# Kernel optimization log

Hardware: AMD Instinct MI355X
Metric: run time of the kernel (lower is better)

The kernel has to match this reference:

```python
import jax, jax.numpy as jnp
import numpy as np

VOCAB, EMBED, TOPICS, NDOCS = 30000, 200, 100, 2048
DT_ALPHA, TW_ALPHA = 3.0, 2.0
EPS_OT = 1e-16   # ETP sinkhorn epsilon
EPS_LOG = 1e-12  # FASTopic self.epsilon
N_SINKHORN_ITERS = 100  # fixed iteration count (original: while err>thr and cpt<max_iter)


def pairwise_sqeuclidean(x, y):
    return (jnp.sum(x * x, axis=1, keepdims=True)
            + jnp.sum(y * y, axis=1)
            - 2.0 * (x @ y.T))


def sinkhorn_etp(x, y, a, b, alpha):
    # Entropic OT between point clouds x:[n,d], y:[m,d]; a:[n,1], b:[m,1] marginals.
    M = pairwise_sqeuclidean(x, y)          # [n, m]
    K = jnp.exp(-alpha * M)                  # Gibbs kernel
    u0 = jnp.full_like(a, 1.0 / a.shape[0])

    def step(carry, _):
        u, _v = carry
        v = b / (K.T @ u + EPS_OT)           # [m,1]
        u = a / (K @ v + EPS_OT)             # [n,1]
        return (u, v), None

    (u, v), _ = jax.lax.scan(step, (u0, jnp.zeros_like(b)), None, length=N_SINKHORN_ITERS)
    transp = u * (K * v.T)                   # [n, m] transport plan
    loss = jnp.sum(transp * M)
    return loss, transp


def setup_inputs() -> dict:
    key = jax.random.key(0)
    k1, k2, k3, k4 = jax.random.split(key, 4)
    # word_embeddings: trunc_normal(std=1) then L2-row-normalize
    we = jax.random.truncated_normal(k1, -2.0, 2.0, (VOCAB, EMBED), jnp.float32)
    we = we / jnp.linalg.norm(we, axis=1, keepdims=True)
    # topic_embeddings: trunc_normal(std=0.1) then L2-row-normalize
    te = 0.1 * jax.random.truncated_normal(k2, -2.0, 2.0, (TOPICS, EMBED), jnp.float32)
    te = te / jnp.linalg.norm(te, axis=1, keepdims=True)
    word_weights = jnp.full((VOCAB, 1), 1.0 / VOCAB, jnp.float32)
    topic_weights = jnp.full((TOPICS, 1), 1.0 / TOPICS, jnp.float32)
    train_bow = jax.random.uniform(k3, (NDOCS, VOCAB), jnp.float32)
    doc_embeddings = jax.random.normal(k4, (NDOCS, EMBED), jnp.float32)
    return {
        "train_bow": train_bow,
        "doc_embeddings": doc_embeddings,
        "word_embeddings": we,
        "topic_embeddings": te,
        "word_weights": word_weights,
        "topic_weights": topic_weights,
    }


def reference(train_bow, doc_embeddings, word_embeddings, topic_embeddings,
              word_weights, topic_weights):
    n_docs = doc_embeddings.shape[0]
    n_topics = topic_embeddings.shape[0]
    # DT_ETP: a uniform over docs, b = softmax(topic_weights)
    a_dt = jnp.full((n_docs, 1), 1.0 / n_docs, doc_embeddings.dtype)
    b_dt = jax.nn.softmax(topic_weights, axis=0)
    loss_DT, transp_DT = sinkhorn_etp(doc_embeddings, topic_embeddings, a_dt, b_dt, DT_ALPHA)
    # TW_ETP: a uniform over topics, b = softmax(word_weights)
    a_tw = jnp.full((n_topics, 1), 1.0 / n_topics, topic_embeddings.dtype)
    b_tw = jax.nn.softmax(word_weights, axis=0)
    loss_TW, transp_TW = sinkhorn_etp(topic_embeddings, word_embeddings, a_tw, b_tw, TW_ALPHA)

    loss_ETP = loss_DT + loss_TW
    theta = transp_DT * n_docs               # [N, K]
    beta = transp_TW * n_topics              # [K, V]
    recon = theta @ beta                     # [N, V]
    loss_DSR = -jnp.mean(jnp.sum(train_bow * jnp.log(recon + EPS_LOG), axis=1))
    loss = loss_DSR + loss_ETP
    return loss, loss_DSR, loss_ETP
```

## Files before the change

kernel.cpp:

```cpp
#include <hip/hip_runtime.h>
#include <math.h>

#define V 30000
#define E 200
#define T 100
#define N 2048
#define NITER 100
#define KSTR 112
#define EPS_OT 1e-16f
#define EPS_LOG 1e-12f

#define OFF_KTW    0
#define OFF_KDT    1680000
#define OFF_WW     1884800
#define OFF_DD     1914800
#define OFF_TT     1916848
#define OFF_PM     1916976
#define OFF_PS     1917104
#define OFF_BTW    1917232
#define OFF_BDT    1947232
#define OFF_ACC    1947360
#define OFF_ACCDT  1957360
#define OFF_VTW    1967360
#define OFF_UDT    1997360
#define OFF_UTW    1999408
#define OFF_VDT    1999536
#define OFF_DBL    1999664
#define OFF_FLAG   1999680
#define OFF_KDTNZ  1999681
#define OFF_ARR    1999682

#define NTW 118
#define NDT 8

#define LOBF(u) __uint_as_float((u) << 16)
#define HIBF(u) __uint_as_float((u) & 0xffff0000u)

__device__ __forceinline__ unsigned short f2bf(float f) {
    unsigned int u = __float_as_uint(f);
    return (unsigned short)((u + 0x7fffu + ((u >> 16) & 1u)) >> 16);
}
__device__ __forceinline__ float bf2f(unsigned short h) {
    return __uint_as_float(((unsigned int)h) << 16);
}

__device__ __forceinline__ float brsum(float x, float* red8) {
    int tid = threadIdx.x;
    for (int o = 32; o; o >>= 1) x += __shfl_down(x, o, 64);
    __syncthreads();
    if ((tid & 63) == 0) red8[tid >> 6] = x;
    __syncthreads();
    return (red8[0] + red8[1]) + (red8[2] + red8[3]);
}

__device__ __forceinline__ void load_krow(const unsigned short* kg, int j, unsigned* ku) {
    const uint4* kp = (const uint4*)(kg + (size_t)j * KSTR);
    #pragma unroll
    for (int i = 0; i < 12; i++) {
        uint4 q = kp[i];
        ku[4*i] = q.x; ku[4*i+1] = q.y; ku[4*i+2] = q.z; ku[4*i+3] = q.w;
    }
    uint2 q2 = *(const uint2*)(((const unsigned*)kp) + 48);
    ku[48] = q2.x; ku[49] = q2.y;
}

__device__ __forceinline__ void gbar(int* ctr, int n, int tid) {
    __syncthreads();
    if (tid == 0) {
        __hip_atomic_fetch_add(ctr, 1, __ATOMIC_RELEASE, __HIP_MEMORY_SCOPE_AGENT);
        while (__hip_atomic_load(ctr, __ATOMIC_ACQUIRE, __HIP_MEMORY_SCOPE_AGENT) < n)
            __builtin_amdgcn_s_sleep(1);
    }
    __syncthreads();
}

__device__ __forceinline__ float agent_ldf(const float* p) {
    return __hip_atomic_load(p, __ATOMIC_RELAXED, __HIP_MEMORY_SCOPE_AGENT);
}

__global__ void k_pre(const float* __restrict__ we, const float* __restrict__ de,
                      const float* __restrict__ te, const float* __restrict__ wwgt,
                      const float* __restrict__ twgt, float* ws) {
    __shared__ float red[256];
    int tid = threadIdx.x, b = blockIdx.x;
    int gid = b * 256 + tid;
    if (gid < 2 * NITER * T) ws[OFF_ACC + gid] = 0.f;
    if (gid < 16) ws[OFF_DBL + gid] = 0.f;
    if (gid < 2) ((int*)ws)[OFF_FLAG + gid] = 0;
    if (gid < 2 * NITER) ((int*)ws)[OFF_ARR + gid] = 0;
    {
        int r = gid;
        const float* src = nullptr; float* dst = nullptr; int row = 0;
        if (r < V)              { src = we; dst = ws + OFF_WW; row = r; }
        else if (r < V + N)     { src = de; dst = ws + OFF_DD; row = r - V; }
        else if (r < V + N + T) { src = te; dst = ws + OFF_TT; row = r - V - N; }
        if (src) {
            const float4* p = (const float4*)(src + (size_t)row * E);
            float s = 0.f;
            #pragma unroll 10
            for (int i = 0; i < E / 4; i++) { float4 v = p[i]; s += v.x*v.x + v.y*v.y + v.z*v.z + v.w*v.w; }
            dst[row] = s;
        }
    }
    if (b < 118) {
        int j = gid;
        float w = (j < V) ? wwgt[j] : -INFINITY;
        red[tid] = w; __syncthreads();
        for (int s = 128; s > 0; s >>= 1) { if (tid < s) red[tid] = fmaxf(red[tid], red[tid + s]); __syncthreads(); }
        float m = red[0]; __syncthreads();
        float e = (j < V) ? expf(w - m) : 0.f;
        red[tid] = e; __syncthreads();
        for (int s = 128; s > 0; s >>= 1) { if (tid < s) red[tid] += red[tid + s]; __syncthreads(); }
        if (tid == 0) { ws[OFF_PM + b] = m; ws[OFF_PS + b] = red[0]; }
    } else if (b == 120) {
        float w = (tid < T) ? twgt[tid] : -INFINITY;
        red[tid] = w; __syncthreads();
        for (int s = 128; s > 0; s >>= 1) { if (tid < s) red[tid] = fmaxf(red[tid], red[tid + s]); __syncthreads(); }
        float m = red[0]; __syncthreads();
        float e = (tid < T) ? expf(w - m) : 0.f;
        red[tid] = e; __syncthreads();
        for (int s = 128; s > 0; s >>= 1) { if (tid < s) red[tid] += red[tid + s]; __syncthreads(); }
        if (tid < T) ws[OFF_BDT + tid] = e / red[0];
    }
}

__global__ void k_pre2(const float* __restrict__ wwgt, float* ws) {
    __shared__ float red[128];
    int tid = threadIdx.x, b = blockIdx.x;
    float m = (tid < 118) ? ws[OFF_PM + tid] : -INFINITY;
    if (tid < 128) red[tid] = m;
    __syncthreads();
    for (int s = 64; s > 0; s >>= 1) { if (tid < s) red[tid] = fmaxf(red[tid], red[tid + s]); __syncthreads(); }
    float mw = red[0]; __syncthreads();
    float p = (tid < 118) ? ws[OFF_PS + tid] * expf(ws[OFF_PM + tid] - mw) : 0.f;
    if (tid < 128) red[tid] = p;
    __syncthreads();
    for (int s = 64; s > 0; s >>= 1) { if (tid < s) red[tid] += red[tid + s]; __syncthreads(); }
    float Sw = red[0];
    int j = b * 256 + tid;
    if (j < V) ws[OFF_BTW + j] = expf(wwgt[j] - mw) / Sw;
}

__global__ void k_ktw(const float* __restrict__ we, const float* __restrict__ te, float* ws) {
    __shared__ float wt[8][256];
    __shared__ float tp[8][25];
    __shared__ float tts[25];
    int tid = threadIdx.x;
    int j0 = blockIdx.x * 256;
    int t0 = blockIdx.y * 25;
    int j = j0 + tid;
    int jl = (j < V) ? j : V - 1;
    float acc[25];
    #pragma unroll
    for (int i = 0; i < 25; i++) acc[i] = 0.f;
    if (tid < 25) tts[tid] = ws[OFF_TT + t0 + tid];
    for (int kk = 0; kk < E; kk += 8) {
        #pragma unroll
        for (int k = 0; k < 8; k++) wt[k][tid] = we[(size_t)jl * E + kk + k];
        if (tid < 200) { int i = tid >> 3; int k = tid & 7; tp[k][i] = te[(size_t)(t0 + i) * E + kk + k]; }
        __syncthreads();
        #pragma unroll
        for (int k = 0; k < 8; k++) {
            float w = wt[k][tid];
            #pragma unroll
            for (int i = 0; i < 25; i++) acc[i] += tp[k][i] * w;
        }
        __syncthreads();
    }
    if (j < V) {
        float wwj = ws[OFF_WW + j];
        unsigned short* kg = (unsigned short*)(ws + OFF_KTW);
        #pragma unroll
        for (int i = 0; i < 25; i++) {
            float M = tts[i] + wwj - 2.f * acc[i];
            kg[(size_t)j * KSTR + t0 + i] = f2bf(expf(-2.f * M));
        }
    }
}

__global__ void k_kdt(const float* __restrict__ de, const float* __restrict__ te, float* ws) {
    int gid = blockIdx.x * 256 + threadIdx.x;
    if (gid >= N * T) return;
    int n = gid / T; int t = gid - n * T;
    const float4* dp  = (const float4*)(de + (size_t)n * E);
    const float4* tpp = (const float4*)(te + (size_t)t * E);
    float s = 0.f;
    #pragma unroll 10
    for (int i = 0; i < E / 4; i++) { float4 a = dp[i], b = tpp[i]; s += a.x*b.x + a.y*b.y + a.z*b.z + a.w*b.w; }
    float M = ws[OFF_DD + n] + ws[OFF_TT + t] - 2.f * s;
    float kv = expf(-3.f * M);
    ws[OFF_KDT + gid] = kv;
    unsigned long long m = __ballot(kv != 0.f);
    if (m && (threadIdx.x & 63) == 0) atomicOr(((int*)ws) + OFF_KDTNZ, 1);
}

__global__ __launch_bounds__(256, 1) void k_sink(const float* __restrict__ bow, float* ws) {
    __shared__ float sm[256 * 26];
    __shared__ float pr[256];
    __shared__ float u_sh[100];
    __shared__ float red8[8];
    int tid = threadIdx.x, b = blockIdx.x;
    int* arr = ((int*)ws) + OFF_ARR;

    if (b >= 118 && b < 246) {
        const float4* b4 = (const float4*)bow;
        for (int k = 0; k < 96; k++) {
            size_t base = (size_t)k * 160000;
            float s = 0.f;
            for (int i = (b - 118) * 256 + tid; i < 160000; i += 128 * 256) {
                float4 x = b4[base + i]; s += (x.x + x.y) + (x.z + x.w);
            }
            float bs = brsum(s, red8);
            if (tid == 0) atomicAdd((double*)(ws + OFF_DBL) + 3, (double)bs);
        }
        return;
    }

    if (b >= 246) {
        if (((volatile int*)ws)[OFF_KDTNZ] == 0) return;
        int d = (b - 246) * 256 + tid;
        const float* Kr = ws + OFF_KDT + (size_t)d * T;
        for (int k = 0; k < NITER; k++) {
            if (tid < T) u_sh[tid] = (k == 0) ? 0.f
                : ws[OFF_BDT + tid] / (agent_ldf(ws + OFF_ACCDT + (k - 1) * T + tid) + EPS_OT);
            __syncthreads();
            float u;
            if (k == 0) u = 1.f / N;
            else {
                float s = 0.f;
                #pragma unroll 4
                for (int t = 0; t < T; t++) s += Kr[t] * u_sh[t];
                u = (1.f / N) / (s + EPS_OT);
            }
            #pragma unroll
            for (int c = 0; c < 4; c++) {
                #pragma unroll
                for (int i = 0; i < 25; i++) sm[tid * 26 + i] = Kr[25 * c + i] * u;
                __syncthreads();
                int g = tid >> 5, tl = tid & 31;
                float s2 = 0.f;
                if (tl < 25) {
                    #pragma unroll 8
                    for (int q = 0; q < 32; q++) s2 += sm[(g * 32 + q) * 26 + tl];
                }
                pr[g * 32 + tl] = s2;
                __syncthreads();
                if (tid < 25) {
                    float r = 0.f;
                    #pragma unroll
                    for (int g2 = 0; g2 < 8; g2++) r += pr[g2 * 32 + tid];
                    atomicAdd(&ws[OFF_ACCDT + k * T + 25 * c + tid], r);
                }
                __syncthreads();
            }
            gbar(arr + NITER + k, NDT, tid);
        }
        if (tid < T) {
            float vf = ws[OFF_BDT + tid] / (agent_ldf(ws + OFF_ACCDT + (NITER - 1) * T + tid) + EPS_OT);
            u_sh[tid] = vf;
            if (b == 246) ws[OFF_VDT + tid] = vf;
        }
        __syncthreads();
        float s = 0.f;
        #pragma unroll 4
        for (int t = 0; t < T; t++) s += Kr[t] * u_sh[t];
        float u = (1.f / N) / (s + EPS_OT);
        ws[OFF_UDT + d] = u;
        float ld = 0.f; int nz = 0;
        for (int t = 0; t < T; t++) {
            float kv = Kr[t];
            if (kv > 0.f) ld += u * kv * u_sh[t] * (-(1.f / 3.f) * logf(kv));
            if ((float)N * u * kv * u_sh[t] != 0.f) nz = 1;
        }
        float ldb = brsum(ld, red8);
        if (tid == 0) atomicAdd((double*)(ws + OFF_DBL) + 1, (double)ldb);
        if (nz) atomicOr(((int*)ws) + OFF_FLAG, 1);
        return;
    }

    const unsigned short* kg = (const unsigned short*)(ws + OFF_KTW);
    int j = b * 256 + tid;
    bool oob = (j >= V);
    int jc = oob ? V - 1 : j;
    unsigned ku[50];
    load_krow(kg, jc, ku);
    if (oob) {
        #pragma unroll
        for (int q = 0; q < 50; q++) ku[q] = 0;
    }
    float bj = oob ? 0.f : ws[OFF_BTW + j];
    float v = 0.f;
    for (int k = 0; k < NITER; k++) {
        if (tid < T) u_sh[tid] = (k == 0) ? 0.01f
            : 0.01f / (agent_ldf(ws + OFF_ACC + (k - 1) * T + tid) + EPS_OT);
        __syncthreads();
        float s = 0.f;
        #pragma unroll
        for (int q = 0; q < 50; q++)
            s += LOBF(ku[q]) * u_sh[2 * q] + HIBF(ku[q]) * u_sh[2 * q + 1];
        v = oob ? 0.f : bj / (s + EPS_OT);
        if (k == NITER - 1 && !oob) ws[OFF_VTW + j] = v;
        __syncthreads();
        #pragma unroll
        for (int c = 0; c < 4; c++) {
            #pragma unroll
            for (int i = 0; i < 25; i++) {
                int t = 25 * c + i;
                unsigned w = ku[t >> 1];
                float kt = (t & 1) ? HIBF(w) : LOBF(w);
                sm[tid * 26 + i] = kt * v;
            }
            __syncthreads();
            int g = tid >> 5, tl = tid & 31;
            float s2 = 0.f;
            if (tl < 25) {
                #pragma unroll 8
                for (int q = 0; q < 32; q++) s2 += sm[(g * 32 + q) * 26 + tl];
            }
            pr[g * 32 + tl] = s2;
            __syncthreads();
            if (tid < 25) {
                float r = 0.f;
                #pragma unroll
                for (int g2 = 0; g2 < 8; g2++) r += pr[g2 * 32 + tid];
                atomicAdd(&ws[OFF_ACC + k * T + 25 * c + tid], r);
            }
            __syncthreads();
        }
        gbar(arr + k, NTW, tid);
    }
    if (tid < T) {
        float a = agent_ldf(ws + OFF_ACC + (NITER - 1) * T + tid);
        float uf = 0.01f / (a + EPS_OT);
        u_sh[tid] = uf;
        if (b == 0) ws[OFF_UTW + tid] = uf;
    }
    __syncthreads();
    float lt = 0.f;
    if (!oob) {
        #pragma unroll
        for (int q = 0; q < 50; q++) {
            float k0 = LOBF(ku[q]), k1 = HIBF(ku[q]);
            if (k0 > 0.f) lt += u_sh[2 * q]     * k0 * v * (-0.5f * logf(k0));
            if (k1 > 0.f) lt += u_sh[2 * q + 1] * k1 * v * (-0.5f * logf(k1));
        }
    }
    float ltb = brsum(lt, red8);
    if (tid == 0) atomicAdd((double*)(ws + OFF_DBL) + 2, (double)ltb);
}

__global__ void k_dsr(const float* __restrict__ bow, float* ws) {
    if (*(volatile int*)(((int*)ws) + OFF_FLAG) == 0) return;
    __shared__ float th[32 * T];
    __shared__ float u2[T];
    __shared__ float vd[T];
    __shared__ float red[256];
    __shared__ int flag;
    int tid = threadIdx.x;
    int j0 = blockIdx.x * 256;
    int d0 = blockIdx.y * 32;
    if (tid < T) { vd[tid] = ws[OFF_VDT + tid]; u2[tid] = ws[OFF_UTW + tid]; }
    if (tid == 0) flag = 0;
    __syncthreads();
    bool nz = false;
    for (int idx = tid; idx < 32 * T; idx += 256) {
        int dl = idx / T; int t = idx - dl * T;
        float thv = (float)N * ws[OFF_UDT + d0 + dl] * ws[OFF_KDT + (size_t)(d0 + dl) * T + t] * vd[t];
        th[idx] = thv;
        nz |= (thv != 0.f);
    }
    if (nz) flag = 1;
    __syncthreads();
    int j = j0 + tid;
    float part = 0.f;
    const unsigned short* kg = (const unsigned short*)(ws + OFF_KTW);
    if (flag) {
        float acc[32];
        #pragma unroll
        for (int d = 0; d < 32; d++) acc[d] = 0.f;
        if (j < V) {
            float vj = ws[OFF_VTW + j];
            for (int t = 0; t < T; t++) {
                float kv = bf2f(kg[(size_t)j * KSTR + t]);
                float beta = (float)T * u2[t] * kv * vj;
                #pragma unroll
                for (int d = 0; d < 32; d++) acc[d] += th[d * T + t] * beta;
            }
            for (int d = 0; d < 32; d++)
                part += bow[(size_t)(d0 + d) * V + j] * logf(acc[d] + EPS_LOG);
        }
    } else {
        if (j < V) {
            float sb = 0.f;
            #pragma unroll 8
            for (int d = 0; d < 32; d++) sb += bow[(size_t)(d0 + d) * V + j];
            part = sb * logf(EPS_LOG);
        }
    }
    red[tid] = part; __syncthreads();
    for (int s = 128; s > 0; s >>= 1) { if (tid < s) red[tid] += red[tid + s]; __syncthreads(); }
    if (tid == 0) atomicAdd((double*)(ws + OFF_DBL) + 0, (double)red[0]);
}

__global__ void k_finish(float* ws, float* out) {
    if (threadIdx.x == 0 && blockIdx.x == 0) {
        double* dbl = (double*)(ws + OFF_DBL);
        int flag = ((int*)ws)[OFF_FLAG];
        double dsr_sum = flag ? dbl[0] : dbl[3] * (double)logf(EPS_LOG);
        double ldsr = -dsr_sum / (double)N;
        double letp = dbl[1] + dbl[2];
        out[0] = (float)(ldsr + letp);
        out[1] = (float)ldsr;
        out[2] = (float)letp;
    }
}

extern "C" void kernel_launch(void* const* d_in, const int* in_sizes, int n_in,
                              void* d_out, int out_size, void* d_ws, size_t ws_size,
                              hipStream_t stream) {
    const float* bow  = (const float*)d_in[0];
    const float* de   = (const float*)d_in[1];
    const float* we   = (const float*)d_in[2];
    const float* te   = (const float*)d_in[3];
    const float* wwgt = (const float*)d_in[4];
    const float* twgt = (const float*)d_in[5];
    float* out = (float*)d_out;
    float* ws  = (float*)d_ws;

    k_pre<<<128, 256, 0, stream>>>(we, de, te, wwgt, twgt, ws);
    k_pre2<<<118, 256, 0, stream>>>(wwgt, ws);
    k_ktw<<<dim3(118, 4), 256, 0, stream>>>(we, te, ws);
    k_kdt<<<800, 256, 0, stream>>>(de, te, ws);
    k_sink<<<254, 256, 0, stream>>>(bow, ws);
    k_dsr<<<dim3(118, 64), 256, 0, stream>>>(bow, ws);
    k_finish<<<1, 64, 0, stream>>>(ws, out);
}
```

Before: 1.395 ms.

## Pack three vocab columns per thread and replace atomics with per-block partials

```diff
diff --git a/kernel.cpp b/kernel.cpp
--- a/kernel.cpp
+++ b/kernel.cpp
@@ -9,6 +9,11 @@
 #define KSTR 112
 #define EPS_OT 1e-16f
 #define EPS_LOG 1e-12f
+
+#define NBTW 40
+#define WPT 3
+#define NDT 8
+#define PBLK 128
 
 #define OFF_KTW    0
 #define OFF_KDT    1680000
@@ -29,9 +34,7 @@
 #define OFF_FLAG   1999680
 #define OFF_KDTNZ  1999681
 #define OFF_ARR    1999682
-
-#define NTW 118
-#define NDT 8
+#define OFF_PART   2000000
 
 #define LOBF(u) __uint_as_float((u) << 16)
 #define HIBF(u) __uint_as_float((u) & 0xffff0000u)
@@ -76,6 +79,9 @@
 
 __device__ __forceinline__ float agent_ldf(const float* p) {
     return __hip_atomic_load(p, __ATOMIC_RELAXED, __HIP_MEMORY_SCOPE_AGENT);
+}
+__device__ __forceinline__ void agent_stf(float* p, float v) {
+    __hip_atomic_store(p, v, __ATOMIC_RELAXED, __HIP_MEMORY_SCOPE_AGENT);
 }
 
 __global__ void k_pre(const float* __restrict__ we, const float* __restrict__ de,
@@ -202,12 +208,12 @@
     int tid = threadIdx.x, b = blockIdx.x;
     int* arr = ((int*)ws) + OFF_ARR;
 
-    if (b >= 118 && b < 246) {
+    if (b >= NBTW && b < NBTW + 128) {
         const float4* b4 = (const float4*)bow;
         for (int k = 0; k < 96; k++) {
             size_t base = (size_t)k * 160000;
             float s = 0.f;
-            for (int i = (b - 118) * 256 + tid; i < 160000; i += 128 * 256) {
+            for (int i = (b - NBTW) * 256 + tid; i < 160000; i += 128 * 256) {
                 float4 x = b4[base + i]; s += (x.x + x.y) + (x.z + x.w);
             }
             float bs = brsum(s, red8);
@@ -216,9 +222,9 @@
         return;
     }
 
-    if (b >= 246) {
+    if (b >= NBTW + 128) {
         if (((volatile int*)ws)[OFF_KDTNZ] == 0) return;
-        int d = (b - 246) * 256 + tid;
+        int d = (b - (NBTW + 128)) * 256 + tid;
         const float* Kr = ws + OFF_KDT + (size_t)d * T;
         for (int k = 0; k < NITER; k++) {
             if (tid < T) u_sh[tid] = (k == 0) ? 0.f
@@ -258,7 +264,7 @@
         if (tid < T) {
             float vf = ws[OFF_BDT + tid] / (agent_ldf(ws + OFF_ACCDT + (NITER - 1) * T + tid) + EPS_OT);
             u_sh[tid] = vf;
-            if (b == 246) ws[OFF_VDT + tid] = vf;
+            if (b == NBTW + 128) ws[OFF_VDT + tid] = vf;
         }
         __syncthreads();
         float s = 0.f;
@@ -279,36 +285,63 @@
     }
 
     const unsigned short* kg = (const unsigned short*)(ws + OFF_KTW);
-    int j = b * 256 + tid;
-    bool oob = (j >= V);
-    int jc = oob ? V - 1 : j;
-    unsigned ku[50];
-    load_krow(kg, jc, ku);
-    if (oob) {
-        #pragma unroll
-        for (int q = 0; q < 50; q++) ku[q] = 0;
-    }
-    float bj = oob ? 0.f : ws[OFF_BTW + j];
-    float v = 0.f;
+    unsigned ku[WPT][50];
+    float bj[WPT];
+    #pragma unroll
+    for (int w = 0; w < WPT; w++) {
+        int j = (b * WPT + w) * 256 + tid;
+        bool oob = (j >= V);
+        load_krow(kg, oob ? V - 1 : j, ku[w]);
+        if (oob) {
+            #pragma unroll
+            for (int q = 0; q < 50; q++) ku[w][q] = 0;
+        }
+        bj[w] = oob ? 0.f : ws[OFF_BTW + j];
+    }
+    float v[WPT];
+    #pragma unroll
+    for (int w = 0; w < WPT; w++) v[w] = 0.f;
+
     for (int k = 0; k < NITER; k++) {
-        if (tid < T) u_sh[tid] = (k == 0) ? 0.01f
-            : 0.01f / (agent_ldf(ws + OFF_ACC + (k - 1) * T + tid) + EPS_OT);
+        if (k == 0) {
+            if (tid < T) u_sh[tid] = 0.01f;
+        } else if (tid < T) {
+            const float* Pp = ws + OFF_PART + (size_t)((k - 1) & 1) * NBTW * PBLK + tid;
+            float a = 0.f;
+            #pragma unroll
+            for (int bb = 0; bb < NBTW; bb++) a += agent_ldf(Pp + bb * PBLK);
+            u_sh[tid] = 0.01f / (a + EPS_OT);
+        }
         __syncthreads();
-        float s = 0.f;
-        #pragma unroll
-        for (int q = 0; q < 50; q++)
-            s += LOBF(ku[q]) * u_sh[2 * q] + HIBF(ku[q]) * u_sh[2 * q + 1];
-        v = oob ? 0.f : bj / (s + EPS_OT);
-        if (k == NITER - 1 && !oob) ws[OFF_VTW + j] = v;
-        __syncthreads();
+        #pragma unroll
+        for (int w = 0; w < WPT; w++) {
+            float s = 0.f;
+            #pragma unroll
+            for (int q = 0; q < 50; q++)
+                s += LOBF(ku[w][q]) * u_sh[2 * q] + HIBF(ku[w][q]) * u_sh[2 * q + 1];
+            v[w] = bj[w] / (s + EPS_OT);
+        }
+        if (k == NITER - 1) {
+            #pragma unroll
+            for (int w = 0; w < WPT; w++) {
+                int j = (b * WPT + w) * 256 + tid;
+                if (j < V) ws[OFF_VTW + j] = v[w];
+            }
+        }
+        float* Pw = ws + OFF_PART + (size_t)(k & 1) * NBTW * PBLK + b * PBLK;
         #pragma unroll
         for (int c = 0; c < 4; c++) {
             #pragma unroll
             for (int i = 0; i < 25; i++) {
                 int t = 25 * c + i;
-                unsigned w = ku[t >> 1];
-                float kt = (t & 1) ? HIBF(w) : LOBF(w);
-                sm[tid * 26 + i] = kt * v;
+                float p = 0.f;
+                #pragma unroll
+                for (int w = 0; w < WPT; w++) {
+                    unsigned wu = ku[w][t >> 1];
+                    float kt = (t & 1) ? HIBF(wu) : LOBF(wu);
+                    p += kt * v[w];
+                }
+                sm[tid * 26 + i] = p;
             }
             __syncthreads();
             int g = tid >> 5, tl = tid & 31;
@@ -323,26 +356,33 @@
                 float r = 0.f;
                 #pragma unroll
                 for (int g2 = 0; g2 < 8; g2++) r += pr[g2 * 32 + tid];
-                atomicAdd(&ws[OFF_ACC + k * T + 25 * c + tid], r);
+                agent_stf(Pw + 25 * c + tid, r);
             }
             __syncthreads();
         }
-        gbar(arr + k, NTW, tid);
+        gbar(arr + k, NBTW, tid);
     }
     if (tid < T) {
-        float a = agent_ldf(ws + OFF_ACC + (NITER - 1) * T + tid);
+        const float* Pp = ws + OFF_PART + (size_t)((NITER - 1) & 1) * NBTW * PBLK + tid;
+        float a = 0.f;
+        #pragma unroll
+        for (int bb = 0; bb < NBTW; bb++) a += agent_ldf(Pp + bb * PBLK);
         float uf = 0.01f / (a + EPS_OT);
         u_sh[tid] = uf;
         if (b == 0) ws[OFF_UTW + tid] = uf;
     }
     __syncthreads();
     float lt = 0.f;
-    if (!oob) {
-        #pragma unroll
-        for (int q = 0; q < 50; q++) {
-            float k0 = LOBF(ku[q]), k1 = HIBF(ku[q]);
-            if (k0 > 0.f) lt += u_sh[2 * q]     * k0 * v * (-0.5f * logf(k0));
-            if (k1 > 0.f) lt += u_sh[2 * q + 1] * k1 * v * (-0.5f * logf(k1));
+    #pragma unroll
+    for (int w = 0; w < WPT; w++) {
+        int j = (b * WPT + w) * 256 + tid;
+        if (j < V) {
+            #pragma unroll
+            for (int q = 0; q < 50; q++) {
+                float k0 = LOBF(ku[w][q]), k1 = HIBF(ku[w][q]);
+                if (k0 > 0.f) lt += u_sh[2 * q]     * k0 * v[w] * (-0.5f * logf(k0));
+                if (k1 > 0.f) lt += u_sh[2 * q + 1] * k1 * v[w] * (-0.5f * logf(k1));
+            }
         }
     }
     float ltb = brsum(lt, red8);
@@ -431,7 +471,7 @@
     k_pre2<<<118, 256, 0, stream>>>(wwgt, ws);
     k_ktw<<<dim3(118, 4), 256, 0, stream>>>(we, te, ws);
     k_kdt<<<800, 256, 0, stream>>>(de, te, ws);
-    k_sink<<<254, 256, 0, stream>>>(bow, ws);
+    k_sink<<<NBTW + 128 + NDT, 256, 0, stream>>>(bow, ws);
     k_dsr<<<dim3(118, 64), 256, 0, stream>>>(bow, ws);
     k_finish<<<1, 64, 0, stream>>>(ws, out);
 }
```

New measurement: 2.078 ms. +49.0%, slower.
